# Kernel tuning notes

Hardware: AMD Instinct MI355X
Metric: run time of the kernel (lower is better)

## Reference

```python
import jax, jax.numpy as jnp
import numpy as np

SEL = [46, 92]
NEURON = [24, 48, 96]
AXIS = 8
NNEI = sum(SEL)            # 138
NDESCRPT = NNEI * 4        # 552
NFRAMES = 32
NATOMS0 = 192
N = NFRAMES * NATOMS0      # 6144 atom rows


def setup_inputs() -> dict:
    key = jax.random.key(0)
    ks = jax.random.split(key, 25)
    inp = {"dmatrix": jax.random.normal(ks[0], (N, NDESCRPT), dtype=jnp.float32)}
    dims = [1] + NEURON
    i = 1
    for t in range(len(SEL)):
        for l in range(len(NEURON)):
            nin, nout = dims[l], dims[l + 1]
            inp[f"w{t}_{l}"] = (jax.random.normal(ks[i], (nin, nout), dtype=jnp.float32)
                                 / np.float32(np.sqrt(nin + nout)))
            i += 1
            inp[f"b{t}_{l}"] = jax.random.normal(ks[i], (1, nout), dtype=jnp.float32)
            i += 1
    inp["nframes"] = NFRAMES
    return inp


def _type_mlp(x, Ws, bs):
    # x: [M, 1] radial channel; ResidualLinear chain 1->24->48->96.
    h = jnp.tanh(x @ Ws[0] + bs[0])                       # 1->24: no residual
    for l in (1, 2):                                      # doubling residual paths
        hn = jnp.tanh(h @ Ws[l] + bs[l])
        h = jnp.concatenate([h, h], axis=-1) + hn
    return h                                              # [M, 96]


def reference(dmatrix, w0_0, b0_0, w0_1, b0_1, w0_2, b0_2,
              w1_0, b1_0, w1_1, b1_1, w1_2, b1_2, nframes):
    params = [((w0_0, w0_1, w0_2), (b0_0, b0_1, b0_2)),
              ((w1_0, w1_1, w1_2), (b1_0, b1_1, b1_2))]
    M = NEURON[-1]
    acc = 0.0
    off = 0
    for t, (Ws, bs) in enumerate(params):
        sel = SEL[t]
        # per-type neighbor slice: [N, sel, 4]
        dd = dmatrix[:, off * 4:(off + sel) * 4].reshape(-1, sel, 4)
        g = _type_mlp(dd[:, :, 0:1].reshape(-1, 1), Ws, bs).reshape(-1, sel, M)
        # [N,4,sel] @ [N,sel,96] -> [N,4,96]
        acc = acc + jnp.einsum('nsd,nse->nde', dd, g)
        off += sel
    xs = acc / np.float32(NNEI)                           # [N, 4, 96]
    # [N,96,4] @ [N,4,axis] -> [N,96,axis]
    res = jnp.einsum('nde,ndk->nek', xs, xs[:, :, :AXIS])
    return res.reshape(nframes, -1)                       # [nframes, natoms0*96*axis]
```

## Files before the change

kernel.cpp:

```cpp
#include <hip/hip_runtime.h>
#include <hip/hip_fp16.h>

typedef _Float16 f16;

__global__ __launch_bounds__(128)
void build_table(const float* __restrict__ w00, const float* __restrict__ b00,
                 const float* __restrict__ w01, const float* __restrict__ b01,
                 const float* __restrict__ w02, const float* __restrict__ b02,
                 const float* __restrict__ w10, const float* __restrict__ b10,
                 const float* __restrict__ w11, const float* __restrict__ b11,
                 const float* __restrict__ w12, const float* __restrict__ b12,
                 f16* __restrict__ tab, int rowsPerType, float xmin, float h)
{
    __shared__ float h0s[8][24];
    __shared__ float h1s[8][48];

    const int ty  = blockIdx.y;
    const int r0  = blockIdx.x * 8;
    const int tid = threadIdx.x;

    const float* __restrict__ W0 = ty ? w10 : w00;
    const float* __restrict__ B0 = ty ? b10 : b00;
    const float* __restrict__ W1 = ty ? w11 : w01;
    const float* __restrict__ B1 = ty ? b11 : b01;
    const float* __restrict__ W2 = ty ? w12 : w02;
    const float* __restrict__ B2 = ty ? b12 : b02;

#pragma unroll
    for (int p = 0; p < 2; ++p) {
        const int idx = p * 128 + tid;
        if (idx < 192) {
            const int q = idx / 24, j = idx - q * 24;
            const float x = __builtin_fmaf((float)(r0 + q), h, xmin);
            h0s[q][j] = tanhf(__builtin_fmaf(x, W0[j], B0[j]));
        }
    }
    __syncthreads();

    if (tid < 96) {
        const int half = tid / 48, k = tid - half * 48;
        float w1c[24];
#pragma unroll
        for (int j = 0; j < 24; ++j) w1c[j] = W1[j * 48 + k];
        const float bk = B1[k];
        const int km = (k < 24) ? k : (k - 24);
#pragma unroll
        for (int qq = 0; qq < 4; ++qq) {
            const int q = half * 4 + qq;
            float a = bk;
#pragma unroll
            for (int j = 0; j < 24; ++j)
                a = __builtin_fmaf(h0s[q][j], w1c[j], a);
            h1s[q][k] = tanhf(a) + h0s[q][km];
        }
    }
    __syncthreads();

    if (tid < 96) {
        const int e = tid;
        float w2c[48];
#pragma unroll
        for (int k = 0; k < 48; ++k) w2c[k] = W2[k * 96 + e];
        const float be = B2[e];
        const int em = (e < 48) ? e : (e - 48);
#pragma unroll
        for (int q = 0; q < 8; ++q) {
            if (r0 + q < rowsPerType) {
                float a = be;
#pragma unroll
                for (int k = 0; k < 48; ++k)
                    a = __builtin_fmaf(h1s[q][k], w2c[k], a);
                tab[((size_t)ty * rowsPerType + r0 + q) * 96 + e] = (f16)(tanhf(a) + h1s[q][em]);
            }
        }
    }
}

__global__ __launch_bounds__(192, 4)
void emb_main(const float* __restrict__ dmat, const f16* __restrict__ tab,
              int nseg, float scale, float offs,
              float* __restrict__ out)
{
    __shared__ float DD[144 * 4];
    __shared__ float Y2s[3 * 4 * 96];

    const int tid = threadIdx.x, n = blockIdx.x;
    const int w = tid >> 6, lane = tid & 63;
    const int l15 = lane & 15, lhi = lane >> 4;

    if (lane < 48) {
        const int t = w + 3 * (lane >> 4);
        const int r = t * 16 + (lane & 15);
        const bool t0 = (t < 3);
        const int  s  = t0 ? r : (r - 2);
        const bool ok = t0 ? (r < 46) : (r < 140);
        float4 v = make_float4(0.f, 0.f, 0.f, 0.f);
        if (ok) v = *reinterpret_cast<const float4*>(dmat + (size_t)n * 552 + s * 4);
        *reinterpret_cast<float4*>(&DD[r * 4]) = v;
    }

    float yp[24];
#pragma unroll
    for (int i = 0; i < 24; ++i) yp[i] = 0.f;

    const float clampHi = (float)nseg - 0.5f;
    const int rowU32 = 48;

    for (int t = w; t < 9; t += 3) {
        const int tyt = (t >= 3);
        const uint32_t* __restrict__ tb =
            reinterpret_cast<const uint32_t*>(tab + (size_t)tyt * (nseg + 1) * 96);

        int irow[4]; float fr[4]; float4 dd4[4];
#pragma unroll
        for (int rg = 0; rg < 4; ++rg) {
            const int r = t * 16 + lhi * 4 + rg;
            const float x = DD[r * 4];
            float u = __builtin_fmaf(x, scale, offs);
            u = fminf(fmaxf(u, 0.f), clampHi);
            const int i = (int)u;
            irow[rg] = i * rowU32;
            fr[rg]   = u - (float)i;
            dd4[rg]  = *reinterpret_cast<const float4*>(&DD[r * 4]);
        }

#pragma unroll
        for (int c = 0; c < 3; ++c) {
#pragma unroll
            for (int rg = 0; rg < 4; ++rg) {
                const uint32_t* p = tb + irow[rg] + c * 16 + l15;
                const uint32_t alo = p[0];
                const uint32_t ahi = p[rowU32];
                const __half2 lo2 = *reinterpret_cast<const __half2*>(&alo);
                const __half2 hi2 = *reinterpret_cast<const __half2*>(&ahi);
                const float2 lo = __half22float2(lo2);
                const float2 hi = __half22float2(hi2);
                const float g0 = __builtin_fmaf(fr[rg], hi.x - lo.x, lo.x);
                const float g1 = __builtin_fmaf(fr[rg], hi.y - lo.y, lo.y);
                const int b = c * 8;
                yp[b + 0] = __builtin_fmaf(dd4[rg].x, g0, yp[b + 0]);
                yp[b + 1] = __builtin_fmaf(dd4[rg].y, g0, yp[b + 1]);
                yp[b + 2] = __builtin_fmaf(dd4[rg].z, g0, yp[b + 2]);
                yp[b + 3] = __builtin_fmaf(dd4[rg].w, g0, yp[b + 3]);
                yp[b + 4] = __builtin_fmaf(dd4[rg].x, g1, yp[b + 4]);
                yp[b + 5] = __builtin_fmaf(dd4[rg].y, g1, yp[b + 5]);
                yp[b + 6] = __builtin_fmaf(dd4[rg].z, g1, yp[b + 6]);
                yp[b + 7] = __builtin_fmaf(dd4[rg].w, g1, yp[b + 7]);
            }
        }
    }

#pragma unroll
    for (int i = 0; i < 24; ++i) {
        float v = yp[i];
        v += __shfl_xor(v, 16);
        v += __shfl_xor(v, 32);
        yp[i] = v;
    }
    if (lhi == 0) {
#pragma unroll
        for (int c = 0; c < 3; ++c)
#pragma unroll
            for (int d = 0; d < 4; ++d) {
                const float2 v2 = make_float2(yp[c * 8 + d], yp[c * 8 + 4 + d]);
                *reinterpret_cast<float2*>(&Y2s[w * 384 + d * 96 + c * 32 + 2 * l15]) = v2;
            }
    }
    __syncthreads();

    if (tid < 96) {
        constexpr float inv = 1.0f / 138.0f;
        const float x0 = (Y2s[tid]       + Y2s[384 + tid]       + Y2s[768 + tid])       * inv;
        const float x1 = (Y2s[96 + tid]  + Y2s[384 + 96 + tid]  + Y2s[768 + 96 + tid])  * inv;
        const float x2 = (Y2s[192 + tid] + Y2s[384 + 192 + tid] + Y2s[768 + 192 + tid]) * inv;
        const float x3 = (Y2s[288 + tid] + Y2s[384 + 288 + tid] + Y2s[768 + 288 + tid]) * inv;
        float rv[8];
#pragma unroll
        for (int k = 0; k < 8; ++k) {
            const float k0 = (Y2s[k]       + Y2s[384 + k]       + Y2s[768 + k])       * inv;
            const float k1 = (Y2s[96 + k]  + Y2s[384 + 96 + k]  + Y2s[768 + 96 + k])  * inv;
            const float k2 = (Y2s[192 + k] + Y2s[384 + 192 + k] + Y2s[768 + 192 + k]) * inv;
            const float k3 = (Y2s[288 + k] + Y2s[384 + 288 + k] + Y2s[768 + 288 + k]) * inv;
            float rr = x0 * k0;
            rr = __builtin_fmaf(x1, k1, rr);
            rr = __builtin_fmaf(x2, k2, rr);
            rr = __builtin_fmaf(x3, k3, rr);
            rv[k] = rr;
        }
        float* op = out + (size_t)n * 768 + tid * 8;
        *reinterpret_cast<float4*>(op)     = make_float4(rv[0], rv[1], rv[2], rv[3]);
        *reinterpret_cast<float4*>(op + 4) = make_float4(rv[4], rv[5], rv[6], rv[7]);
    }
}

extern "C" void kernel_launch(void* const* d_in, const int* in_sizes, int n_in,
                              void* d_out, int out_size, void* d_ws, size_t ws_size,
                              hipStream_t stream)
{
    const float* dmat = (const float*)d_in[0];
    const int n_atoms = in_sizes[0] / 552;

    int nseg = 1024;
    while ((size_t)2 * (size_t)(nseg + 1) * 96 * sizeof(f16) > ws_size && nseg > 16)
        nseg >>= 1;
    const float xmin = -8.f, xmax = 8.f;
    const float h     = (xmax - xmin) / (float)nseg;
    const float scale = (float)nseg / (xmax - xmin);
    const float offs  = -xmin * scale;
    f16* tab = (f16*)d_ws;

    const int rowsPerType = nseg + 1;
    dim3 bgrid((rowsPerType + 7) / 8, 2);
    build_table<<<bgrid, 128, 0, stream>>>(
        (const float*)d_in[1],  (const float*)d_in[2],
        (const float*)d_in[3],  (const float*)d_in[4],
        (const float*)d_in[5],  (const float*)d_in[6],
        (const float*)d_in[7],  (const float*)d_in[8],
        (const float*)d_in[9],  (const float*)d_in[10],
        (const float*)d_in[11], (const float*)d_in[12],
        tab, rowsPerType, xmin, h);

    emb_main<<<n_atoms, 192, 0, stream>>>(dmat, tab, nseg, scale, offs, (float*)d_out);
}
```

Measured before the change: 40.39 us.

## Process two atoms per block and interpolate table entries in packed half2

Each block now handles two atom rows, so the per-block setup, reduction and epilogue costs are amortised and the final 192 threads all do useful output work. Table interpolation uses packed half2 arithmetic instead of converting both endpoints to float first. In exchange, register pressure roughly doubles with two accumulator sets, the grid assumes an even atom count, and half-precision interpolation loses some accuracy.

```diff
diff --git a/kernel.cpp b/kernel.cpp
--- a/kernel.cpp
+++ b/kernel.cpp
@@ -81,12 +81,13 @@
               int nseg, float scale, float offs,
               float* __restrict__ out)
 {
-    __shared__ float DD[144 * 4];
-    __shared__ float Y2s[3 * 4 * 96];
-
-    const int tid = threadIdx.x, n = blockIdx.x;
+    __shared__ float DD[2][144 * 4];
+    __shared__ float Y2s[2][3 * 4 * 96];
+
+    const int tid = threadIdx.x;
     const int w = tid >> 6, lane = tid & 63;
     const int l15 = lane & 15, lhi = lane >> 4;
+    const int nA = blockIdx.x * 2, nB = nA + 1;
 
     if (lane < 48) {
         const int t = w + 3 * (lane >> 4);
@@ -94,100 +95,150 @@
         const bool t0 = (t < 3);
         const int  s  = t0 ? r : (r - 2);
         const bool ok = t0 ? (r < 46) : (r < 140);
-        float4 v = make_float4(0.f, 0.f, 0.f, 0.f);
-        if (ok) v = *reinterpret_cast<const float4*>(dmat + (size_t)n * 552 + s * 4);
-        *reinterpret_cast<float4*>(&DD[r * 4]) = v;
-    }
-
-    float yp[24];
-#pragma unroll
-    for (int i = 0; i < 24; ++i) yp[i] = 0.f;
+        float4 vA = make_float4(0.f, 0.f, 0.f, 0.f);
+        float4 vB = make_float4(0.f, 0.f, 0.f, 0.f);
+        if (ok) {
+            vA = *reinterpret_cast<const float4*>(dmat + (size_t)nA * 552 + s * 4);
+            vB = *reinterpret_cast<const float4*>(dmat + (size_t)nB * 552 + s * 4);
+        }
+        *reinterpret_cast<float4*>(&DD[0][r * 4]) = vA;
+        *reinterpret_cast<float4*>(&DD[1][r * 4]) = vB;
+    }
+
+    float ypA[24], ypB[24];
+#pragma unroll
+    for (int i = 0; i < 24; ++i) { ypA[i] = 0.f; ypB[i] = 0.f; }
 
     const float clampHi = (float)nseg - 0.5f;
     const int rowU32 = 48;
 
-    for (int t = w; t < 9; t += 3) {
+#pragma unroll
+    for (int it = 0; it < 3; ++it) {
+        const int t = w + 3 * it;
         const int tyt = (t >= 3);
         const uint32_t* __restrict__ tb =
             reinterpret_cast<const uint32_t*>(tab + (size_t)tyt * (nseg + 1) * 96);
 
-        int irow[4]; float fr[4]; float4 dd4[4];
+        int irowA[4], irowB[4];
+        __half2 frA[4], frB[4];
+        float4 ddA[4], ddB[4];
 #pragma unroll
         for (int rg = 0; rg < 4; ++rg) {
             const int r = t * 16 + lhi * 4 + rg;
-            const float x = DD[r * 4];
-            float u = __builtin_fmaf(x, scale, offs);
-            u = fminf(fmaxf(u, 0.f), clampHi);
-            const int i = (int)u;
-            irow[rg] = i * rowU32;
-            fr[rg]   = u - (float)i;
-            dd4[rg]  = *reinterpret_cast<const float4*>(&DD[r * 4]);
+            {
+                const float x = DD[0][r * 4];
+                float u = __builtin_fmaf(x, scale, offs);
+                u = fminf(fmaxf(u, 0.f), clampHi);
+                const int i = (int)u;
+                irowA[rg] = i * rowU32;
+                const float fr = u - (float)i;
+                frA[rg] = __float2half2_rn(fr);
+                ddA[rg] = *reinterpret_cast<const float4*>(&DD[0][r * 4]);
+            }
+            {
+                const float x = DD[1][r * 4];
+                float u = __builtin_fmaf(x, scale, offs);
+                u = fminf(fmaxf(u, 0.f), clampHi);
+                const int i = (int)u;
+                irowB[rg] = i * rowU32;
+                const float fr = u - (float)i;
+                frB[rg] = __float2half2_rn(fr);
+                ddB[rg] = *reinterpret_cast<const float4*>(&DD[1][r * 4]);
+            }
         }
 
 #pragma unroll
         for (int c = 0; c < 3; ++c) {
+            const int b = c * 8;
 #pragma unroll
             for (int rg = 0; rg < 4; ++rg) {
-                const uint32_t* p = tb + irow[rg] + c * 16 + l15;
-                const uint32_t alo = p[0];
-                const uint32_t ahi = p[rowU32];
-                const __half2 lo2 = *reinterpret_cast<const __half2*>(&alo);
-                const __half2 hi2 = *reinterpret_cast<const __half2*>(&ahi);
-                const float2 lo = __half22float2(lo2);
-                const float2 hi = __half22float2(hi2);
-                const float g0 = __builtin_fmaf(fr[rg], hi.x - lo.x, lo.x);
-                const float g1 = __builtin_fmaf(fr[rg], hi.y - lo.y, lo.y);
-                const int b = c * 8;
-                yp[b + 0] = __builtin_fmaf(dd4[rg].x, g0, yp[b + 0]);
-                yp[b + 1] = __builtin_fmaf(dd4[rg].y, g0, yp[b + 1]);
-                yp[b + 2] = __builtin_fmaf(dd4[rg].z, g0, yp[b + 2]);
-                yp[b + 3] = __builtin_fmaf(dd4[rg].w, g0, yp[b + 3]);
-                yp[b + 4] = __builtin_fmaf(dd4[rg].x, g1, yp[b + 4]);
-                yp[b + 5] = __builtin_fmaf(dd4[rg].y, g1, yp[b + 5]);
-                yp[b + 6] = __builtin_fmaf(dd4[rg].z, g1, yp[b + 6]);
-                yp[b + 7] = __builtin_fmaf(dd4[rg].w, g1, yp[b + 7]);
+                {
+                    const uint32_t* p = tb + irowA[rg] + c * 16 + l15;
+                    const uint32_t alo = p[0];
+                    const uint32_t ahi = p[rowU32];
+                    const __half2 lo2 = *reinterpret_cast<const __half2*>(&alo);
+                    const __half2 hi2 = *reinterpret_cast<const __half2*>(&ahi);
+                    const __half2 g2 = __hfma2(frA[rg], __hsub2(hi2, lo2), lo2);
+                    const float g0 = __low2float(g2);
+                    const float g1 = __high2float(g2);
+                    ypA[b + 0] = __builtin_fmaf(ddA[rg].x, g0, ypA[b + 0]);
+                    ypA[b + 1] = __builtin_fmaf(ddA[rg].y, g0, ypA[b + 1]);
+                    ypA[b + 2] = __builtin_fmaf(ddA[rg].z, g0, ypA[b + 2]);
+                    ypA[b + 3] = __builtin_fmaf(ddA[rg].w, g0, ypA[b + 3]);
+                    ypA[b + 4] = __builtin_fmaf(ddA[rg].x, g1, ypA[b + 4]);
+                    ypA[b + 5] = __builtin_fmaf(ddA[rg].y, g1, ypA[b + 5]);
+                    ypA[b + 6] = __builtin_fmaf(ddA[rg].z, g1, ypA[b + 6]);
+                    ypA[b + 7] = __builtin_fmaf(ddA[rg].w, g1, ypA[b + 7]);
+                }
+                {
+                    const uint32_t* p = tb + irowB[rg] + c * 16 + l15;
+                    const uint32_t alo = p[0];
+                    const uint32_t ahi = p[rowU32];
+                    const __half2 lo2 = *reinterpret_cast<const __half2*>(&alo);
+                    const __half2 hi2 = *reinterpret_cast<const __half2*>(&ahi);
+                    const __half2 g2 = __hfma2(frB[rg], __hsub2(hi2, lo2), lo2);
+                    const float g0 = __low2float(g2);
+                    const float g1 = __high2float(g2);
+                    ypB[b + 0] = __builtin_fmaf(ddB[rg].x, g0, ypB[b + 0]);
+                    ypB[b + 1] = __builtin_fmaf(ddB[rg].y, g0, ypB[b + 1]);
+                    ypB[b + 2] = __builtin_fmaf(ddB[rg].z, g0, ypB[b + 2]);
+                    ypB[b + 3] = __builtin_fmaf(ddB[rg].w, g0, ypB[b + 3]);
+                    ypB[b + 4] = __builtin_fmaf(ddB[rg].x, g1, ypB[b + 4]);
+                    ypB[b + 5] = __builtin_fmaf(ddB[rg].y, g1, ypB[b + 5]);
+                    ypB[b + 6] = __builtin_fmaf(ddB[rg].z, g1, ypB[b + 6]);
+                    ypB[b + 7] = __builtin_fmaf(ddB[rg].w, g1, ypB[b + 7]);
+                }
             }
         }
     }
 
 #pragma unroll
     for (int i = 0; i < 24; ++i) {
-        float v = yp[i];
-        v += __shfl_xor(v, 16);
-        v += __shfl_xor(v, 32);
-        yp[i] = v;
+        float vA = ypA[i];
+        vA += __shfl_xor(vA, 16);
+        vA += __shfl_xor(vA, 32);
+        ypA[i] = vA;
+        float vB = ypB[i];
+        vB += __shfl_xor(vB, 16);
+        vB += __shfl_xor(vB, 32);
+        ypB[i] = vB;
     }
     if (lhi == 0) {
 #pragma unroll
         for (int c = 0; c < 3; ++c)
 #pragma unroll
             for (int d = 0; d < 4; ++d) {
-                const float2 v2 = make_float2(yp[c * 8 + d], yp[c * 8 + 4 + d]);
-                *reinterpret_cast<float2*>(&Y2s[w * 384 + d * 96 + c * 32 + 2 * l15]) = v2;
+                *reinterpret_cast<float2*>(&Y2s[0][w * 384 + d * 96 + c * 32 + 2 * l15]) =
+                    make_float2(ypA[c * 8 + d], ypA[c * 8 + 4 + d]);
+                *reinterpret_cast<float2*>(&Y2s[1][w * 384 + d * 96 + c * 32 + 2 * l15]) =
+                    make_float2(ypB[c * 8 + d], ypB[c * 8 + 4 + d]);
             }
     }
     __syncthreads();
 
-    if (tid < 96) {
+    {
+        const int at = tid / 96;
+        const int e  = tid - at * 96;
+        const float* Y = Y2s[at];
         constexpr float inv = 1.0f / 138.0f;
-        const float x0 = (Y2s[tid]       + Y2s[384 + tid]       + Y2s[768 + tid])       * inv;
-        const float x1 = (Y2s[96 + tid]  + Y2s[384 + 96 + tid]  + Y2s[768 + 96 + tid])  * inv;
-        const float x2 = (Y2s[192 + tid] + Y2s[384 + 192 + tid] + Y2s[768 + 192 + tid]) * inv;
-        const float x3 = (Y2s[288 + tid] + Y2s[384 + 288 + tid] + Y2s[768 + 288 + tid]) * inv;
+        const float x0 = (Y[e]       + Y[384 + e]       + Y[768 + e])       * inv;
+        const float x1 = (Y[96 + e]  + Y[384 + 96 + e]  + Y[768 + 96 + e])  * inv;
+        const float x2 = (Y[192 + e] + Y[384 + 192 + e] + Y[768 + 192 + e]) * inv;
+        const float x3 = (Y[288 + e] + Y[384 + 288 + e] + Y[768 + 288 + e]) * inv;
         float rv[8];
 #pragma unroll
         for (int k = 0; k < 8; ++k) {
-            const float k0 = (Y2s[k]       + Y2s[384 + k]       + Y2s[768 + k])       * inv;
-            const float k1 = (Y2s[96 + k]  + Y2s[384 + 96 + k]  + Y2s[768 + 96 + k])  * inv;
-            const float k2 = (Y2s[192 + k] + Y2s[384 + 192 + k] + Y2s[768 + 192 + k]) * inv;
-            const float k3 = (Y2s[288 + k] + Y2s[384 + 288 + k] + Y2s[768 + 288 + k]) * inv;
+            const float k0 = (Y[k]       + Y[384 + k]       + Y[768 + k])       * inv;
+            const float k1 = (Y[96 + k]  + Y[384 + 96 + k]  + Y[768 + 96 + k])  * inv;
+            const float k2 = (Y[192 + k] + Y[384 + 192 + k] + Y[768 + 192 + k]) * inv;
+            const float k3 = (Y[288 + k] + Y[384 + 288 + k] + Y[768 + 288 + k]) * inv;
             float rr = x0 * k0;
             rr = __builtin_fmaf(x1, k1, rr);
             rr = __builtin_fmaf(x2, k2, rr);
             rr = __builtin_fmaf(x3, k3, rr);
             rv[k] = rr;
         }
-        float* op = out + (size_t)n * 768 + tid * 8;
+        float* op = out + (size_t)(nA + at) * 768 + e * 8;
         *reinterpret_cast<float4*>(op)     = make_float4(rv[0], rv[1], rv[2], rv[3]);
         *reinterpret_cast<float4*>(op + 4) = make_float4(rv[4], rv[5], rv[6], rv[7]);
     }
@@ -220,5 +271,5 @@
         (const float*)d_in[11], (const float*)d_in[12],
         tab, rowsPerType, xmin, h);
 
-    emb_main<<<n_atoms, 192, 0, stream>>>(dmat, tab, nseg, scale, offs, (float*)d_out);
+    emb_main<<<n_atoms / 2, 192, 0, stream>>>(dmat, tab, nseg, scale, offs, (float*)d_out);
 }
```

Measured after the change: 41.52 us. +2.8%, slower.
